# Performance work log

Hardware: AMD Instinct MI355X
Metric: run time of the kernel (lower is better)

## Reference

```python
import jax, jax.numpy as jnp
import numpy as np

N_NODES = 50000


def _gcn_norm(edge_index, num_nodes):
    # add self-loops (PyG GCNConv default)
    loop = jnp.arange(num_nodes, dtype=edge_index.dtype)
    src = jnp.concatenate([edge_index[0], loop])
    dst = jnp.concatenate([edge_index[1], loop])
    deg = jax.ops.segment_sum(jnp.ones_like(dst, dtype=jnp.float32), dst,
                              num_segments=num_nodes)
    dis = jnp.where(deg > 0, jax.lax.rsqrt(deg), 0.0)  # deg^{-1/2}
    norm = dis[src] * dis[dst]                          # [E+N]
    return src, dst, norm


def _gcn_conv(x, W, b, src, dst, norm, num_nodes):
    h = x @ W                                   # [N, out] transform first
    msg = h[src] * norm[:, None]                # gather + scale  [E+N, out]
    out = jax.ops.segment_sum(msg, dst, num_segments=num_nodes)  # scatter-add
    return out + b


def setup_inputs() -> dict:
    key = jax.random.key(0)
    k1, k2, k3, k4, k5 = jax.random.split(key, 5)
    in_dim, hid_dim, out_dim = 128, 64, 2
    x = jax.random.normal(k1, (N_NODES, in_dim), dtype=jnp.float32)
    edge_index = jax.random.randint(k2, (2, 800000), 0, N_NODES, dtype=jnp.int64)
    s1 = 1.0 / np.sqrt(in_dim)
    s2 = 1.0 / np.sqrt(hid_dim)
    W1 = jax.random.uniform(k3, (in_dim, hid_dim), jnp.float32, -s1, s1)
    b1 = jnp.zeros((hid_dim,), jnp.float32)
    W2 = jax.random.uniform(k4, (hid_dim, hid_dim), jnp.float32, -s2, s2)
    b2 = jnp.zeros((hid_dim,), jnp.float32)
    Wl = jax.random.uniform(k5, (hid_dim, out_dim), jnp.float32, -s2, s2)
    bl = jnp.zeros((out_dim,), jnp.float32)
    return {"x": x, "edge_index": edge_index, "W1": W1, "b1": b1,
            "W2": W2, "b2": b2, "Wl": Wl, "bl": bl}


def reference(x, edge_index, W1, b1, W2, b2, Wl, bl):
    num_nodes = x.shape[0]
    src, dst, norm = _gcn_norm(edge_index, num_nodes)
    h = _gcn_conv(x, W1, b1, src, dst, norm, num_nodes)
    h = jax.nn.relu(h)
    # dropout is identity at inference
    h = _gcn_conv(h, W2, b2, src, dst, norm, num_nodes)
    h = jax.nn.relu(h)
    logits = h @ Wl + bl
    return logits
```

## Files before the change

### kernel.cpp

```cpp
#include <hip/hip_runtime.h>

#define IN_DIM 128
#define HID 64
#define STAGE_CAP 12288

__global__ void k_init(int* __restrict__ deg, int* __restrict__ gcur, int N) {
    int i = blockIdx.x * blockDim.x + threadIdx.x;
    if (i < N) deg[i] = 0;
    if (i < 256) gcur[i] = 0;
}

__global__ void k_count(const int* __restrict__ dst, int E, int* __restrict__ deg) {
    int e = blockIdx.x * blockDim.x + threadIdx.x;
    if (e < E) atomicAdd(&deg[dst[e]], 1);
}

__global__ __launch_bounds__(256) void k_scan_part(const int* __restrict__ deg, int N,
                                                   int* __restrict__ bsum) {
    int tid = threadIdx.x;
    int i = blockIdx.x * 256 + tid;
    int v = (i < N) ? deg[i] : 0;
    int lane = tid & 63, wid = tid >> 6;
    for (int off = 32; off; off >>= 1) v += __shfl_down(v, off);
    __shared__ int ws[4];
    if (lane == 0) ws[wid] = v;
    __syncthreads();
    if (tid == 0) bsum[blockIdx.x] = ws[0] + ws[1] + ws[2] + ws[3];
}

__global__ __launch_bounds__(256) void k_scan_top(int* __restrict__ bsum, int nb,
                                                  int* __restrict__ row_start, int N) {
    int tid = threadIdx.x;
    int lane = tid & 63, wid = tid >> 6;
    int v = (tid < nb) ? bsum[tid] : 0;
    int orig = v;
    for (int off = 1; off < 64; off <<= 1) {
        int t = __shfl_up(v, off);
        if (lane >= off) v += t;
    }
    __shared__ int ws[4];
    if (lane == 63) ws[wid] = v;
    __syncthreads();
    int woff = 0;
    for (int w = 0; w < 4; ++w)
        if (w < wid) woff += ws[w];
    if (tid < nb) bsum[tid] = woff + v - orig;
    if (tid == 0) row_start[N] = ws[0] + ws[1] + ws[2] + ws[3];
}

__global__ __launch_bounds__(256) void k_scan_final(const int* __restrict__ deg,
                                                    const int* __restrict__ bsum, int N,
                                                    int* __restrict__ row_start,
                                                    float* __restrict__ dis) {
    int tid = threadIdx.x;
    int i = blockIdx.x * 256 + tid;
    int v = (i < N) ? deg[i] : 0;
    int orig = v;
    int lane = tid & 63, wid = tid >> 6;
    for (int off = 1; off < 64; off <<= 1) {
        int t = __shfl_up(v, off);
        if (lane >= off) v += t;
    }
    __shared__ int ws[4];
    if (lane == 63) ws[wid] = v;
    __syncthreads();
    int woff = 0;
    for (int w = 0; w < 4; ++w)
        if (w < wid) woff += ws[w];
    if (i < N) {
        row_start[i] = bsum[blockIdx.x] + woff + v - orig;
        dis[i] = rsqrtf((float)(orig + 1));
    }
}

__global__ __launch_bounds__(512) void k_bin_scatter(const int* __restrict__ src,
                                                     const int* __restrict__ dst, int E,
                                                     const int* __restrict__ row_start,
                                                     int* __restrict__ gcur,
                                                     unsigned* __restrict__ ebuf) {
    __shared__ int hist[256];
    __shared__ int gbase[256];
    int tid = threadIdx.x;
    for (int i = tid; i < 256; i += 512) hist[i] = 0;
    __syncthreads();
    int base = blockIdx.x * 4096;
    int pk[8], bkt[8], rnk[8];
#pragma unroll
    for (int i = 0; i < 8; ++i) {
        int e = base + tid + i * 512;
        if (e < E) {
            int s = src[e];
            int d = dst[e];
            bkt[i] = d >> 8;
            pk[i] = ((d & 255) << 16) | s;
            rnk[i] = atomicAdd(&hist[bkt[i]], 1);
        } else {
            bkt[i] = -1;
        }
    }
    __syncthreads();
    for (int b = tid; b < 256; b += 512) {
        int c = hist[b];
        if (c > 0) gbase[b] = row_start[b << 8] + atomicAdd(&gcur[b], c);
    }
    __syncthreads();
#pragma unroll
    for (int i = 0; i < 8; ++i) {
        if (bkt[i] >= 0) ebuf[gbase[bkt[i]] + rnk[i]] = (unsigned)pk[i];
    }
}

__global__ __launch_bounds__(512) void k_bin_sort(const unsigned* __restrict__ ebuf,
                                                  const int* __restrict__ row_start, int N,
                                                  int* __restrict__ csr_src) {
    __shared__ int lrs[257];
    __shared__ int lcur[256];
    __shared__ unsigned short stage[STAGE_CAP];
    int tid = threadIdx.x;
    int node0 = blockIdx.x << 8;
    int nnode = min(256, N - node0);
    for (int i = tid; i <= nnode; i += 512) lrs[i] = row_start[node0 + i];
    for (int i = tid; i < nnode; i += 512) lcur[i] = 0;
    __syncthreads();
    int bstart = lrs[0], bend = lrs[nnode];
    int cnt = bend - bstart;
    if (cnt <= STAGE_CAP) {
        for (int i = tid; i < cnt; i += 512) {
            unsigned u = ebuf[bstart + i];
            int dlo = (u >> 16) & 255;
            int pos = (lrs[dlo] - bstart) + atomicAdd(&lcur[dlo], 1);
            stage[pos] = (unsigned short)(u & 0xFFFF);
        }
        __syncthreads();
        for (int i = tid; i < cnt; i += 512) csr_src[bstart + i] = (int)stage[i];
    } else {
        for (int i = tid; i < cnt; i += 512) {
            unsigned u = ebuf[bstart + i];
            int dlo = (u >> 16) & 255;
            int pos = lrs[dlo] + atomicAdd(&lcur[dlo], 1);
            csr_src[pos] = (int)(u & 0xFFFF);
        }
    }
}

template <int K>
__global__ __launch_bounds__(256) void k_gemm_scale(const float* __restrict__ X,
                                                    const float* __restrict__ W,
                                                    const float* __restrict__ dis, int N,
                                                    float* __restrict__ out) {
    constexpr int KP = K + 4;
    constexpr int KC = K / 4;
    __shared__ float Xs[64 * KP];
    __shared__ float Ws[K * 64];
    int tid = threadIdx.x;
    int row0 = blockIdx.x * 64;

    const float4* Wg = (const float4*)W;
    float4* Ws4 = (float4*)Ws;
    for (int i = tid; i < K * 16; i += 256) Ws4[i] = Wg[i];
    const float4* Xg = (const float4*)X;
    for (int c = tid; c < 64 * KC; c += 256) {
        int r = c / KC, k4 = c % KC;
        int row = row0 + r;
        float4 vv = make_float4(0.f, 0.f, 0.f, 0.f);
        if (row < N) vv = Xg[(size_t)row * KC + k4];
        *(float4*)&Xs[r * KP + k4 * 4] = vv;
    }
    __syncthreads();

    int cg = tid & 15;
    int rg = tid >> 4;
    float acc[4][4] = {};
#pragma unroll 2
    for (int k = 0; k < K; k += 4) {
        float4 w0 = *(float4*)&Ws[(k + 0) * 64 + cg * 4];
        float4 w1 = *(float4*)&Ws[(k + 1) * 64 + cg * 4];
        float4 w2 = *(float4*)&Ws[(k + 2) * 64 + cg * 4];
        float4 w3 = *(float4*)&Ws[(k + 3) * 64 + cg * 4];
#pragma unroll
        for (int i = 0; i < 4; ++i) {
            float4 xv = *(float4*)&Xs[(rg * 4 + i) * KP + k];
            acc[i][0] += xv.x * w0.x + xv.y * w1.x + xv.z * w2.x + xv.w * w3.x;
            acc[i][1] += xv.x * w0.y + xv.y * w1.y + xv.z * w2.y + xv.w * w3.y;
            acc[i][2] += xv.x * w0.z + xv.y * w1.z + xv.z * w2.z + xv.w * w3.z;
            acc[i][3] += xv.x * w0.w + xv.y * w1.w + xv.z * w2.w + xv.w * w3.w;
        }
    }
#pragma unroll
    for (int i = 0; i < 4; ++i) {
        int row = row0 + rg * 4 + i;
        if (row < N) {
            float s = dis[row];
            *(float4*)&out[(size_t)row * 64 + cg * 4] =
                make_float4(acc[i][0] * s, acc[i][1] * s, acc[i][2] * s, acc[i][3] * s);
        }
    }
}

__global__ __launch_bounds__(256) void k_aggregate(const float* __restrict__ Hs,
                                                   const int* __restrict__ row_start,
                                                   const int* __restrict__ csr_src,
                                                   const float* __restrict__ dis,
                                                   const float* __restrict__ bias, int N,
                                                   float* __restrict__ out) {
    const float4* Hs4 = (const float4*)Hs;
    int wave = threadIdx.x >> 6, lane = threadIdx.x & 63;
    int node = blockIdx.x * 4 + wave;
    if (node >= N) return;
    int t = lane & 7, g = lane >> 3;
    float4 a0 = make_float4(0.f, 0.f, 0.f, 0.f);
    float4 a1 = make_float4(0.f, 0.f, 0.f, 0.f);
    if (g == 0) {
        a0 = Hs4[(size_t)node * 16 + t];
        a1 = Hs4[(size_t)node * 16 + t + 8];
    }
    int e0 = row_start[node], e1 = row_start[node + 1];
    for (int eb = e0; eb < e1; eb += 64) {
        int cnt = min(64, e1 - eb);
        int sv = (eb + lane < e1) ? csr_src[eb + lane] : 0;
        for (int jb = 0; jb < cnt; jb += 8) {
            int idx = jb + g;
            int s = __shfl(sv, idx);
            float4 z0 = Hs4[(size_t)s * 16 + t];
            float4 z1 = Hs4[(size_t)s * 16 + t + 8];
            if (idx < cnt) {
                a0.x += z0.x; a0.y += z0.y; a0.z += z0.z; a0.w += z0.w;
                a1.x += z1.x; a1.y += z1.y; a1.z += z1.z; a1.w += z1.w;
            }
        }
    }
#pragma unroll
    for (int off = 8; off < 64; off <<= 1) {
        a0.x += __shfl_xor(a0.x, off); a0.y += __shfl_xor(a0.y, off);
        a0.z += __shfl_xor(a0.z, off); a0.w += __shfl_xor(a0.w, off);
        a1.x += __shfl_xor(a1.x, off); a1.y += __shfl_xor(a1.y, off);
        a1.z += __shfl_xor(a1.z, off); a1.w += __shfl_xor(a1.w, off);
    }
    float sc = dis[node];
    const float4* b4 = (const float4*)bias;
    float4 b0 = b4[t], b1 = b4[t + 8];
    float4 v0, v1;
    v0.x = fmaxf(a0.x * sc + b0.x, 0.f); v0.y = fmaxf(a0.y * sc + b0.y, 0.f);
    v0.z = fmaxf(a0.z * sc + b0.z, 0.f); v0.w = fmaxf(a0.w * sc + b0.w, 0.f);
    v1.x = fmaxf(a1.x * sc + b1.x, 0.f); v1.y = fmaxf(a1.y * sc + b1.y, 0.f);
    v1.z = fmaxf(a1.z * sc + b1.z, 0.f); v1.w = fmaxf(a1.w * sc + b1.w, 0.f);
    if (g == 0) ((float4*)out)[(size_t)node * 16 + t] = v0;
    if (g == 1) ((float4*)out)[(size_t)node * 16 + t + 8] = v1;
}

__global__ __launch_bounds__(256) void k_aggregate_head(const float* __restrict__ Hs,
                                                        const int* __restrict__ row_start,
                                                        const int* __restrict__ csr_src,
                                                        const float* __restrict__ dis,
                                                        const float* __restrict__ bias,
                                                        const float* __restrict__ Wl,
                                                        const float* __restrict__ bl, int N,
                                                        float* __restrict__ out) {
    const float4* Hs4 = (const float4*)Hs;
    int wave = threadIdx.x >> 6, lane = threadIdx.x & 63;
    int node = blockIdx.x * 4 + wave;
    if (node >= N) return;
    int t = lane & 7, g = lane >> 3;
    float4 a0 = make_float4(0.f, 0.f, 0.f, 0.f);
    float4 a1 = make_float4(0.f, 0.f, 0.f, 0.f);
    if (g == 0) {
        a0 = Hs4[(size_t)node * 16 + t];
        a1 = Hs4[(size_t)node * 16 + t + 8];
    }
    int e0 = row_start[node], e1 = row_start[node + 1];
    for (int eb = e0; eb < e1; eb += 64) {
        int cnt = min(64, e1 - eb);
        int sv = (eb + lane < e1) ? csr_src[eb + lane] : 0;
        for (int jb = 0; jb < cnt; jb += 8) {
            int idx = jb + g;
            int s = __shfl(sv, idx);
            float4 z0 = Hs4[(size_t)s * 16 + t];
            float4 z1 = Hs4[(size_t)s * 16 + t + 8];
            if (idx < cnt) {
                a0.x += z0.x; a0.y += z0.y; a0.z += z0.z; a0.w += z0.w;
                a1.x += z1.x; a1.y += z1.y; a1.z += z1.z; a1.w += z1.w;
            }
        }
    }
#pragma unroll
    for (int off = 8; off < 64; off <<= 1) {
        a0.x += __shfl_xor(a0.x, off); a0.y += __shfl_xor(a0.y, off);
        a0.z += __shfl_xor(a0.z, off); a0.w += __shfl_xor(a0.w, off);
        a1.x += __shfl_xor(a1.x, off); a1.y += __shfl_xor(a1.y, off);
        a1.z += __shfl_xor(a1.z, off); a1.w += __shfl_xor(a1.w, off);
    }
    float sc = dis[node];
    const float4* b4 = (const float4*)bias;
    float4 b0 = b4[t], b1 = b4[t + 8];
    float4 v0, v1;
    v0.x = fmaxf(a0.x * sc + b0.x, 0.f); v0.y = fmaxf(a0.y * sc + b0.y, 0.f);
    v0.z = fmaxf(a0.z * sc + b0.z, 0.f); v0.w = fmaxf(a0.w * sc + b0.w, 0.f);
    v1.x = fmaxf(a1.x * sc + b1.x, 0.f); v1.y = fmaxf(a1.y * sc + b1.y, 0.f);
    v1.z = fmaxf(a1.z * sc + b1.z, 0.f); v1.w = fmaxf(a1.w * sc + b1.w, 0.f);
    int c0 = 4 * t, c1 = 32 + 4 * t;
    float p0 = v0.x * Wl[(c0 + 0) * 2] + v0.y * Wl[(c0 + 1) * 2] +
               v0.z * Wl[(c0 + 2) * 2] + v0.w * Wl[(c0 + 3) * 2] +
               v1.x * Wl[(c1 + 0) * 2] + v1.y * Wl[(c1 + 1) * 2] +
               v1.z * Wl[(c1 + 2) * 2] + v1.w * Wl[(c1 + 3) * 2];
    float p1 = v0.x * Wl[(c0 + 0) * 2 + 1] + v0.y * Wl[(c0 + 1) * 2 + 1] +
               v0.z * Wl[(c0 + 2) * 2 + 1] + v0.w * Wl[(c0 + 3) * 2 + 1] +
               v1.x * Wl[(c1 + 0) * 2 + 1] + v1.y * Wl[(c1 + 1) * 2 + 1] +
               v1.z * Wl[(c1 + 2) * 2 + 1] + v1.w * Wl[(c1 + 3) * 2 + 1];
    p0 += __shfl_xor(p0, 1); p1 += __shfl_xor(p1, 1);
    p0 += __shfl_xor(p0, 2); p1 += __shfl_xor(p1, 2);
    p0 += __shfl_xor(p0, 4); p1 += __shfl_xor(p1, 4);
    if (lane == 0) {
        out[node * 2 + 0] = p0 + bl[0];
        out[node * 2 + 1] = p1 + bl[1];
    }
}

extern "C" void kernel_launch(void* const* d_in, const int* in_sizes, int n_in,
                              void* d_out, int out_size, void* d_ws, size_t ws_size,
                              hipStream_t stream) {
    const float* x  = (const float*)d_in[0];
    const int*   ei = (const int*)d_in[1];
    const float* W1 = (const float*)d_in[2];
    const float* b1 = (const float*)d_in[3];
    const float* W2 = (const float*)d_in[4];
    const float* b2 = (const float*)d_in[5];
    const float* Wl = (const float*)d_in[6];
    const float* bl = (const float*)d_in[7];

    const int N = in_sizes[0] / IN_DIM;
    const int E = in_sizes[1] / 2;
    const int* src = ei;
    const int* dst = ei + E;

    char* ws = (char*)d_ws;
    size_t off = 0;
    auto alloc = [&](size_t bytes) -> void* {
        void* p = ws + off;
        off = (off + bytes + 255) & ~(size_t)255;
        return p;
    };
    int*   deg       = (int*)alloc((size_t)N * 4);
    int*   row_start = (int*)alloc(((size_t)N + 1) * 4);
    int*   gcur      = (int*)alloc(256 * 4);
    int*   csr_src   = (int*)alloc((size_t)E * 4);
    float* dis       = (float*)alloc((size_t)N * 4);
    int*   bsum      = (int*)alloc(1024 * 4);
    float* bufA      = (float*)alloc((size_t)N * HID * 4);
    float* bufB      = (float*)alloc((size_t)N * HID * 4);
    unsigned* ebuf   = (unsigned*)bufA;

    int nb = (N + 255) / 256;
    k_init<<<nb, 256, 0, stream>>>(deg, gcur, N);
    k_count<<<(E + 255) / 256, 256, 0, stream>>>(dst, E, deg);
    k_scan_part<<<nb, 256, 0, stream>>>(deg, N, bsum);
    k_scan_top<<<1, 256, 0, stream>>>(bsum, nb, row_start, N);
    k_scan_final<<<nb, 256, 0, stream>>>(deg, bsum, N, row_start, dis);
    k_bin_scatter<<<(E + 4095) / 4096, 512, 0, stream>>>(src, dst, E, row_start, gcur, ebuf);
    k_bin_sort<<<nb, 512, 0, stream>>>(ebuf, row_start, N, csr_src);

    int gblk = (N + 63) / 64;
    int nblk = (N + 3) / 4;
    k_gemm_scale<IN_DIM><<<gblk, 256, 0, stream>>>(x, W1, dis, N, bufA);
    k_aggregate<<<nblk, 256, 0, stream>>>(bufA, row_start, csr_src, dis, b1, N, bufB);
    k_gemm_scale<HID><<<gblk, 256, 0, stream>>>(bufB, W2, dis, N, bufA);
    k_aggregate_head<<<nblk, 256, 0, stream>>>(bufA, row_start, csr_src, dis, b2, Wl, bl, N,
                                               (float*)d_out);
}
```

Measured before the change: 168.6 us.

## Build CSR with bucket-level counts and per-bucket local degree scan; widen aggregate gather

Replaces the per-node global atomic degree count and three-pass node scan with a 256-bucket histogram using shared-memory atomics and a single-block bucket scan. Per-node degrees, row_start and dis are now computed inside the bin-sort kernel from the bucketed edges. Separately, the aggregation kernels now give each lane four float4 loads, so 16 edges are handled per iteration with direct csr_src loads instead of shuffles. This drops several launches and the global atomics on deg, at the cost of an extra pass over ebuf in bin_sort and more registers per lane in aggregation.

```diff
diff --git a/kernel.cpp b/kernel.cpp
--- a/kernel.cpp
+++ b/kernel.cpp
@@ -4,36 +4,25 @@
 #define HID 64
 #define STAGE_CAP 12288
 
-__global__ void k_init(int* __restrict__ deg, int* __restrict__ gcur, int N) {
-    int i = blockIdx.x * blockDim.x + threadIdx.x;
-    if (i < N) deg[i] = 0;
-    if (i < 256) gcur[i] = 0;
-}
-
-__global__ void k_count(const int* __restrict__ dst, int E, int* __restrict__ deg) {
-    int e = blockIdx.x * blockDim.x + threadIdx.x;
-    if (e < E) atomicAdd(&deg[dst[e]], 1);
-}
-
-__global__ __launch_bounds__(256) void k_scan_part(const int* __restrict__ deg, int N,
-                                                   int* __restrict__ bsum) {
+__global__ __launch_bounds__(256) void k_bin_count(const int* __restrict__ dst, int E,
+                                                   int* __restrict__ bcnt) {
+    __shared__ int h[256];
     int tid = threadIdx.x;
-    int i = blockIdx.x * 256 + tid;
-    int v = (i < N) ? deg[i] : 0;
-    int lane = tid & 63, wid = tid >> 6;
-    for (int off = 32; off; off >>= 1) v += __shfl_down(v, off);
-    __shared__ int ws[4];
-    if (lane == 0) ws[wid] = v;
-    __syncthreads();
-    if (tid == 0) bsum[blockIdx.x] = ws[0] + ws[1] + ws[2] + ws[3];
-}
-
-__global__ __launch_bounds__(256) void k_scan_top(int* __restrict__ bsum, int nb,
-                                                  int* __restrict__ row_start, int N) {
-    int tid = threadIdx.x;
-    int lane = tid & 63, wid = tid >> 6;
-    int v = (tid < nb) ? bsum[tid] : 0;
-    int orig = v;
+    h[tid] = 0;
+    __syncthreads();
+    int base = blockIdx.x * 4096;
+    int end = min(base + 4096, E);
+    for (int i = base + tid; i < end; i += 256) atomicAdd(&h[dst[i] >> 8], 1);
+    __syncthreads();
+    if (h[tid]) atomicAdd(&bcnt[tid], h[tid]);
+}
+
+__global__ __launch_bounds__(256) void k_bucket_scan(const int* __restrict__ bcnt,
+                                                     int* __restrict__ bbase,
+                                                     int* __restrict__ gcur,
+                                                     int* __restrict__ row_start, int N, int E) {
+    int tid = threadIdx.x, lane = tid & 63, wid = tid >> 6;
+    int v = bcnt[tid], orig = v;
     for (int off = 1; off < 64; off <<= 1) {
         int t = __shfl_up(v, off);
         if (lane >= off) v += t;
@@ -42,40 +31,15 @@
     if (lane == 63) ws[wid] = v;
     __syncthreads();
     int woff = 0;
-    for (int w = 0; w < 4; ++w)
-        if (w < wid) woff += ws[w];
-    if (tid < nb) bsum[tid] = woff + v - orig;
-    if (tid == 0) row_start[N] = ws[0] + ws[1] + ws[2] + ws[3];
-}
-
-__global__ __launch_bounds__(256) void k_scan_final(const int* __restrict__ deg,
-                                                    const int* __restrict__ bsum, int N,
-                                                    int* __restrict__ row_start,
-                                                    float* __restrict__ dis) {
-    int tid = threadIdx.x;
-    int i = blockIdx.x * 256 + tid;
-    int v = (i < N) ? deg[i] : 0;
-    int orig = v;
-    int lane = tid & 63, wid = tid >> 6;
-    for (int off = 1; off < 64; off <<= 1) {
-        int t = __shfl_up(v, off);
-        if (lane >= off) v += t;
-    }
-    __shared__ int ws[4];
-    if (lane == 63) ws[wid] = v;
-    __syncthreads();
-    int woff = 0;
-    for (int w = 0; w < 4; ++w)
-        if (w < wid) woff += ws[w];
-    if (i < N) {
-        row_start[i] = bsum[blockIdx.x] + woff + v - orig;
-        dis[i] = rsqrtf((float)(orig + 1));
-    }
+    for (int w = 0; w < wid; ++w) woff += ws[w];
+    bbase[tid] = woff + v - orig;
+    gcur[tid] = 0;
+    if (tid == 0) row_start[N] = E;
 }
 
 __global__ __launch_bounds__(512) void k_bin_scatter(const int* __restrict__ src,
                                                      const int* __restrict__ dst, int E,
-                                                     const int* __restrict__ row_start,
+                                                     const int* __restrict__ bbase,
                                                      int* __restrict__ gcur,
                                                      unsigned* __restrict__ ebuf) {
     __shared__ int hist[256];
@@ -101,7 +65,7 @@
     __syncthreads();
     for (int b = tid; b < 256; b += 512) {
         int c = hist[b];
-        if (c > 0) gbase[b] = row_start[b << 8] + atomicAdd(&gcur[b], c);
+        if (c > 0) gbase[b] = bbase[b] + atomicAdd(&gcur[b], c);
     }
     __syncthreads();
 #pragma unroll
@@ -111,24 +75,59 @@
 }
 
 __global__ __launch_bounds__(512) void k_bin_sort(const unsigned* __restrict__ ebuf,
-                                                  const int* __restrict__ row_start, int N,
+                                                  const int* __restrict__ bbase, int N, int E,
+                                                  int* __restrict__ row_start,
+                                                  float* __restrict__ dis,
                                                   int* __restrict__ csr_src) {
-    __shared__ int lrs[257];
+    __shared__ int ldeg[256];
+    __shared__ int loff[256];
     __shared__ int lcur[256];
+    __shared__ int wsum[8];
     __shared__ unsigned short stage[STAGE_CAP];
     int tid = threadIdx.x;
     int node0 = blockIdx.x << 8;
     int nnode = min(256, N - node0);
-    for (int i = tid; i <= nnode; i += 512) lrs[i] = row_start[node0 + i];
-    for (int i = tid; i < nnode; i += 512) lcur[i] = 0;
-    __syncthreads();
-    int bstart = lrs[0], bend = lrs[nnode];
+    for (int i = tid; i < 256; i += 512) {
+        ldeg[i] = 0;
+        lcur[i] = 0;
+    }
+    __syncthreads();
+    int bstart = bbase[blockIdx.x];
+    int bend = bbase[blockIdx.x + 1];
     int cnt = bend - bstart;
+    for (int i = tid; i < cnt; i += 512) {
+        unsigned u = ebuf[bstart + i];
+        atomicAdd(&ldeg[(u >> 16) & 255], 1);
+    }
+    __syncthreads();
+    int lane = tid & 63, wid = tid >> 6;
+    int v = 0, orig = 0;
+    if (tid < 256) {
+        orig = ldeg[tid];
+        v = orig;
+    }
+    for (int off = 1; off < 64; off <<= 1) {
+        int t = __shfl_up(v, off);
+        if (lane >= off) v += t;
+    }
+    if (lane == 63) wsum[wid] = v;
+    __syncthreads();
+    if (tid < 256) {
+        int woff = 0;
+        for (int w = 0; w < wid && w < 4; ++w) woff += wsum[w];
+        int excl = woff + v - orig;
+        loff[tid] = excl;
+        if (tid < nnode) {
+            row_start[node0 + tid] = bstart + excl;
+            dis[node0 + tid] = rsqrtf((float)(orig + 1));
+        }
+    }
+    __syncthreads();
     if (cnt <= STAGE_CAP) {
         for (int i = tid; i < cnt; i += 512) {
             unsigned u = ebuf[bstart + i];
             int dlo = (u >> 16) & 255;
-            int pos = (lrs[dlo] - bstart) + atomicAdd(&lcur[dlo], 1);
+            int pos = loff[dlo] + atomicAdd(&lcur[dlo], 1);
             stage[pos] = (unsigned short)(u & 0xFFFF);
         }
         __syncthreads();
@@ -137,7 +136,7 @@
         for (int i = tid; i < cnt; i += 512) {
             unsigned u = ebuf[bstart + i];
             int dlo = (u >> 16) & 255;
-            int pos = lrs[dlo] + atomicAdd(&lcur[dlo], 1);
+            int pos = bstart + loff[dlo] + atomicAdd(&lcur[dlo], 1);
             csr_src[pos] = (int)(u & 0xFFFF);
         }
     }
@@ -207,45 +206,62 @@
     int wave = threadIdx.x >> 6, lane = threadIdx.x & 63;
     int node = blockIdx.x * 4 + wave;
     if (node >= N) return;
-    int t = lane & 7, g = lane >> 3;
+    int t = lane & 3, g = lane >> 2;
     float4 a0 = make_float4(0.f, 0.f, 0.f, 0.f);
-    float4 a1 = make_float4(0.f, 0.f, 0.f, 0.f);
+    float4 a1 = a0, a2 = a0, a3 = a0;
     if (g == 0) {
         a0 = Hs4[(size_t)node * 16 + t];
-        a1 = Hs4[(size_t)node * 16 + t + 8];
+        a1 = Hs4[(size_t)node * 16 + t + 4];
+        a2 = Hs4[(size_t)node * 16 + t + 8];
+        a3 = Hs4[(size_t)node * 16 + t + 12];
     }
     int e0 = row_start[node], e1 = row_start[node + 1];
-    for (int eb = e0; eb < e1; eb += 64) {
-        int cnt = min(64, e1 - eb);
-        int sv = (eb + lane < e1) ? csr_src[eb + lane] : 0;
-        for (int jb = 0; jb < cnt; jb += 8) {
-            int idx = jb + g;
-            int s = __shfl(sv, idx);
-            float4 z0 = Hs4[(size_t)s * 16 + t];
-            float4 z1 = Hs4[(size_t)s * 16 + t + 8];
-            if (idx < cnt) {
-                a0.x += z0.x; a0.y += z0.y; a0.z += z0.z; a0.w += z0.w;
-                a1.x += z1.x; a1.y += z1.y; a1.z += z1.z; a1.w += z1.w;
-            }
-        }
-    }
-#pragma unroll
-    for (int off = 8; off < 64; off <<= 1) {
+    for (int eb = e0; eb < e1; eb += 16) {
+        int idx = eb + g;
+        bool ok = idx < e1;
+        int s = csr_src[ok ? idx : e0];
+        size_t base = (size_t)s * 16;
+        float4 z0 = Hs4[base + t];
+        float4 z1 = Hs4[base + t + 4];
+        float4 z2 = Hs4[base + t + 8];
+        float4 z3 = Hs4[base + t + 12];
+        if (ok) {
+            a0.x += z0.x; a0.y += z0.y; a0.z += z0.z; a0.w += z0.w;
+            a1.x += z1.x; a1.y += z1.y; a1.z += z1.z; a1.w += z1.w;
+            a2.x += z2.x; a2.y += z2.y; a2.z += z2.z; a2.w += z2.w;
+            a3.x += z3.x; a3.y += z3.y; a3.z += z3.z; a3.w += z3.w;
+        }
+    }
+#pragma unroll
+    for (int off = 4; off < 64; off <<= 1) {
         a0.x += __shfl_xor(a0.x, off); a0.y += __shfl_xor(a0.y, off);
         a0.z += __shfl_xor(a0.z, off); a0.w += __shfl_xor(a0.w, off);
         a1.x += __shfl_xor(a1.x, off); a1.y += __shfl_xor(a1.y, off);
         a1.z += __shfl_xor(a1.z, off); a1.w += __shfl_xor(a1.w, off);
+        a2.x += __shfl_xor(a2.x, off); a2.y += __shfl_xor(a2.y, off);
+        a2.z += __shfl_xor(a2.z, off); a2.w += __shfl_xor(a2.w, off);
+        a3.x += __shfl_xor(a3.x, off); a3.y += __shfl_xor(a3.y, off);
+        a3.z += __shfl_xor(a3.z, off); a3.w += __shfl_xor(a3.w, off);
     }
     float sc = dis[node];
     const float4* b4 = (const float4*)bias;
-    float4 b0 = b4[t], b1 = b4[t + 8];
-    float4 v0, v1;
+    float4 b0 = b4[t], b1 = b4[t + 4], b2 = b4[t + 8], b3 = b4[t + 12];
+    float4 v0, v1, v2, v3;
     v0.x = fmaxf(a0.x * sc + b0.x, 0.f); v0.y = fmaxf(a0.y * sc + b0.y, 0.f);
     v0.z = fmaxf(a0.z * sc + b0.z, 0.f); v0.w = fmaxf(a0.w * sc + b0.w, 0.f);
     v1.x = fmaxf(a1.x * sc + b1.x, 0.f); v1.y = fmaxf(a1.y * sc + b1.y, 0.f);
     v1.z = fmaxf(a1.z * sc + b1.z, 0.f); v1.w = fmaxf(a1.w * sc + b1.w, 0.f);
-    if (g == 0) ((float4*)out)[(size_t)node * 16 + t] = v0;
-    if (g == 1) ((float4*)out)[(size_t)node * 16 + t + 8] = v1;
+    v2.x = fmaxf(a2.x * sc + b2.x, 0.f); v2.y = fmaxf(a2.y * sc + b2.y, 0.f);
+    v2.z = fmaxf(a2.z * sc + b2.z, 0.f); v2.w = fmaxf(a2.w * sc + b2.w, 0.f);
+    v3.x = fmaxf(a3.x * sc + b3.x, 0.f); v3.y = fmaxf(a3.y * sc + b3.y, 0.f);
+    v3.z = fmaxf(a3.z * sc + b3.z, 0.f); v3.w = fmaxf(a3.w * sc + b3.w, 0.f);
+    if (g == 0) {
+        float4* o4 = (float4*)out;
+        o4[(size_t)node * 16 + t] = v0;
+        o4[(size_t)node * 16 + t + 4] = v1;
+        o4[(size_t)node * 16 + t + 8] = v2;
+        o4[(size_t)node * 16 + t + 12] = v3;
+    }
 }
 
 __global__ __launch_bounds__(256) void k_aggregate_head(const float* __restrict__ Hs,
@@ -260,55 +276,74 @@
     int wave = threadIdx.x >> 6, lane = threadIdx.x & 63;
     int node = blockIdx.x * 4 + wave;
     if (node >= N) return;
-    int t = lane & 7, g = lane >> 3;
+    int t = lane & 3, g = lane >> 2;
     float4 a0 = make_float4(0.f, 0.f, 0.f, 0.f);
-    float4 a1 = make_float4(0.f, 0.f, 0.f, 0.f);
+    float4 a1 = a0, a2 = a0, a3 = a0;
     if (g == 0) {
         a0 = Hs4[(size_t)node * 16 + t];
-        a1 = Hs4[(size_t)node * 16 + t + 8];
+        a1 = Hs4[(size_t)node * 16 + t + 4];
+        a2 = Hs4[(size_t)node * 16 + t + 8];
+        a3 = Hs4[(size_t)node * 16 + t + 12];
     }
     int e0 = row_start[node], e1 = row_start[node + 1];
-    for (int eb = e0; eb < e1; eb += 64) {
-        int cnt = min(64, e1 - eb);
-        int sv = (eb + lane < e1) ? csr_src[eb + lane] : 0;
-        for (int jb = 0; jb < cnt; jb += 8) {
-            int idx = jb + g;
-            int s = __shfl(sv, idx);
-            float4 z0 = Hs4[(size_t)s * 16 + t];
-            float4 z1 = Hs4[(size_t)s * 16 + t + 8];
-            if (idx < cnt) {
-                a0.x += z0.x; a0.y += z0.y; a0.z += z0.z; a0.w += z0.w;
-                a1.x += z1.x; a1.y += z1.y; a1.z += z1.z; a1.w += z1.w;
-            }
-        }
-    }
-#pragma unroll
-    for (int off = 8; off < 64; off <<= 1) {
+    for (int eb = e0; eb < e1; eb += 16) {
+        int idx = eb + g;
+        bool ok = idx < e1;
+        int s = csr_src[ok ? idx : e0];
+        size_t base = (size_t)s * 16;
+        float4 z0 = Hs4[base + t];
+        float4 z1 = Hs4[base + t + 4];
+        float4 z2 = Hs4[base + t + 8];
+        float4 z3 = Hs4[base + t + 12];
+        if (ok) {
+            a0.x += z0.x; a0.y += z0.y; a0.z += z0.z; a0.w += z0.w;
+            a1.x += z1.x; a1.y += z1.y; a1.z += z1.z; a1.w += z1.w;
+            a2.x += z2.x; a2.y += z2.y; a2.z += z2.z; a2.w += z2.w;
+            a3.x += z3.x; a3.y += z3.y; a3.z += z3.z; a3.w += z3.w;
+        }
+    }
+#pragma unroll
+    for (int off = 4; off < 64; off <<= 1) {
         a0.x += __shfl_xor(a0.x, off); a0.y += __shfl_xor(a0.y, off);
         a0.z += __shfl_xor(a0.z, off); a0.w += __shfl_xor(a0.w, off);
         a1.x += __shfl_xor(a1.x, off); a1.y += __shfl_xor(a1.y, off);
         a1.z += __shfl_xor(a1.z, off); a1.w += __shfl_xor(a1.w, off);
+        a2.x += __shfl_xor(a2.x, off); a2.y += __shfl_xor(a2.y, off);
+        a2.z += __shfl_xor(a2.z, off); a2.w += __shfl_xor(a2.w, off);
+        a3.x += __shfl_xor(a3.x, off); a3.y += __shfl_xor(a3.y, off);
+        a3.z += __shfl_xor(a3.z, off); a3.w += __shfl_xor(a3.w, off);
     }
     float sc = dis[node];
     const float4* b4 = (const float4*)bias;
-    float4 b0 = b4[t], b1 = b4[t + 8];
-    float4 v0, v1;
+    float4 b0 = b4[t], b1 = b4[t + 4], b2 = b4[t + 8], b3 = b4[t + 12];
+    float4 v0, v1, v2, v3;
     v0.x = fmaxf(a0.x * sc + b0.x, 0.f); v0.y = fmaxf(a0.y * sc + b0.y, 0.f);
     v0.z = fmaxf(a0.z * sc + b0.z, 0.f); v0.w = fmaxf(a0.w * sc + b0.w, 0.f);
     v1.x = fmaxf(a1.x * sc + b1.x, 0.f); v1.y = fmaxf(a1.y * sc + b1.y, 0.f);
     v1.z = fmaxf(a1.z * sc + b1.z, 0.f); v1.w = fmaxf(a1.w * sc + b1.w, 0.f);
-    int c0 = 4 * t, c1 = 32 + 4 * t;
+    v2.x = fmaxf(a2.x * sc + b2.x, 0.f); v2.y = fmaxf(a2.y * sc + b2.y, 0.f);
+    v2.z = fmaxf(a2.z * sc + b2.z, 0.f); v2.w = fmaxf(a2.w * sc + b2.w, 0.f);
+    v3.x = fmaxf(a3.x * sc + b3.x, 0.f); v3.y = fmaxf(a3.y * sc + b3.y, 0.f);
+    v3.z = fmaxf(a3.z * sc + b3.z, 0.f); v3.w = fmaxf(a3.w * sc + b3.w, 0.f);
+    int c0 = 4 * t, c1 = 4 * (t + 4), c2 = 4 * (t + 8), c3 = 4 * (t + 12);
     float p0 = v0.x * Wl[(c0 + 0) * 2] + v0.y * Wl[(c0 + 1) * 2] +
                v0.z * Wl[(c0 + 2) * 2] + v0.w * Wl[(c0 + 3) * 2] +
                v1.x * Wl[(c1 + 0) * 2] + v1.y * Wl[(c1 + 1) * 2] +
-               v1.z * Wl[(c1 + 2) * 2] + v1.w * Wl[(c1 + 3) * 2];
+               v1.z * Wl[(c1 + 2) * 2] + v1.w * Wl[(c1 + 3) * 2] +
+               v2.x * Wl[(c2 + 0) * 2] + v2.y * Wl[(c2 + 1) * 2] +
+               v2.z * Wl[(c2 + 2) * 2] + v2.w * Wl[(c2 + 3) * 2] +
+               v3.x * Wl[(c3 + 0) * 2] + v3.y * Wl[(c3 + 1) * 2] +
+               v3.z * Wl[(c3 + 2) * 2] + v3.w * Wl[(c3 + 3) * 2];
     float p1 = v0.x * Wl[(c0 + 0) * 2 + 1] + v0.y * Wl[(c0 + 1) * 2 + 1] +
                v0.z * Wl[(c0 + 2) * 2 + 1] + v0.w * Wl[(c0 + 3) * 2 + 1] +
                v1.x * Wl[(c1 + 0) * 2 + 1] + v1.y * Wl[(c1 + 1) * 2 + 1] +
-               v1.z * Wl[(c1 + 2) * 2 + 1] + v1.w * Wl[(c1 + 3) * 2 + 1];
+               v1.z * Wl[(c1 + 2) * 2 + 1] + v1.w * Wl[(c1 + 3) * 2 + 1] +
+               v2.x * Wl[(c2 + 0) * 2 + 1] + v2.y * Wl[(c2 + 1) * 2 + 1] +
+               v2.z * Wl[(c2 + 2) * 2 + 1] + v2.w * Wl[(c2 + 3) * 2 + 1] +
+               v3.x * Wl[(c3 + 0) * 2 + 1] + v3.y * Wl[(c3 + 1) * 2 + 1] +
+               v3.z * Wl[(c3 + 2) * 2 + 1] + v3.w * Wl[(c3 + 3) * 2 + 1];
     p0 += __shfl_xor(p0, 1); p1 += __shfl_xor(p1, 1);
     p0 += __shfl_xor(p0, 2); p1 += __shfl_xor(p1, 2);
-    p0 += __shfl_xor(p0, 4); p1 += __shfl_xor(p1, 4);
     if (lane == 0) {
         out[node * 2 + 0] = p0 + bl[0];
         out[node * 2 + 1] = p1 + bl[1];
@@ -339,24 +374,24 @@
         off = (off + bytes + 255) & ~(size_t)255;
         return p;
     };
-    int*   deg       = (int*)alloc((size_t)N * 4);
+    int*   bcnt      = (int*)alloc(256 * 4);
+    int*   bbase     = (int*)alloc(257 * 4);
+    int*   gcur      = (int*)alloc(256 * 4);
     int*   row_start = (int*)alloc(((size_t)N + 1) * 4);
-    int*   gcur      = (int*)alloc(256 * 4);
+    float* dis       = (float*)alloc((size_t)N * 4);
     int*   csr_src   = (int*)alloc((size_t)E * 4);
-    float* dis       = (float*)alloc((size_t)N * 4);
-    int*   bsum      = (int*)alloc(1024 * 4);
     float* bufA      = (float*)alloc((size_t)N * HID * 4);
     float* bufB      = (float*)alloc((size_t)N * HID * 4);
     unsigned* ebuf   = (unsigned*)bufA;
 
+    hipMemsetAsync(bcnt, 0, 256 * 4, stream);
+
+    int eblk = (E + 4095) / 4096;
     int nb = (N + 255) / 256;
-    k_init<<<nb, 256, 0, stream>>>(deg, gcur, N);
-    k_count<<<(E + 255) / 256, 256, 0, stream>>>(dst, E, deg);
-    k_scan_part<<<nb, 256, 0, stream>>>(deg, N, bsum);
-    k_scan_top<<<1, 256, 0, stream>>>(bsum, nb, row_start, N);
-    k_scan_final<<<nb, 256, 0, stream>>>(deg, bsum, N, row_start, dis);
-    k_bin_scatter<<<(E + 4095) / 4096, 512, 0, stream>>>(src, dst, E, row_start, gcur, ebuf);
-    k_bin_sort<<<nb, 512, 0, stream>>>(ebuf, row_start, N, csr_src);
+    k_bin_count<<<eblk, 256, 0, stream>>>(dst, E, bcnt);
+    k_bucket_scan<<<1, 256, 0, stream>>>(bcnt, bbase, gcur, row_start, N, E);
+    k_bin_scatter<<<eblk, 512, 0, stream>>>(src, dst, E, bbase, gcur, ebuf);
+    k_bin_sort<<<nb, 512, 0, stream>>>(ebuf, bbase, N, E, row_start, dis, csr_src);
 
     int gblk = (N + 63) / 64;
     int nblk = (N + 3) / 4;
```

Result: faster. 153.3 us (-9.0%).
